# Kernel tuning notes

Measured on AMD Instinct MI355X. Metric: run time of the kernel, lower is better.

Reference implementation:

```python
import jax, jax.numpy as jnp
import numpy as np

B, T, C, H, NC = 512, 256, 512, 512, 96  # batch, encoder steps, channels, hidden, num classes


def setup_inputs() -> dict:
    key = jax.random.key(0)
    ks = jax.random.split(key, 12)
    def w(k, shape, fan):
        return (jax.random.normal(k, shape, jnp.float32) / np.sqrt(fan)).astype(jnp.float32)
    labels = jax.random.randint(ks[0], (B,), 0, NC)
    return {
        "prev_h": jax.random.normal(ks[1], (B, H), jnp.float32),
        "prev_c": jax.random.normal(ks[2], (B, H), jnp.float32),
        "batch_H": jax.random.normal(ks[3], (B, T, C), jnp.float32),
        "char_onehots": jax.nn.one_hot(labels, NC, dtype=jnp.float32),
        "Wi": w(ks[4], (C, H), C),            # i2h kernel (no bias)
        "Wh": w(ks[5], (H, H), H),            # h2h kernel
        "bh": jnp.zeros((H,), jnp.float32),    # h2h bias
        "Ws": w(ks[6], (H, 1), H),            # score kernel (no bias)
        "K": w(ks[7], (C + NC, 4 * H), C + NC),  # LSTM input kernel (i,f,g,o)
        "R": w(ks[8], (H, 4 * H), H),            # LSTM recurrent kernel
        "b": jnp.zeros((4 * H,), jnp.float32),    # LSTM bias
    }


def reference(prev_h, prev_c, batch_H, char_onehots, Wi, Wh, bh, Ws, K, R, b):
    # Additive (Bahdanau) attention
    proj = jnp.einsum('btc,ch->bth', batch_H, Wi)                  # [B,T,H]
    hp = prev_h @ Wh + bh                                          # [B,H]
    e = jnp.einsum('bth,h->bt', jnp.tanh(proj + hp[:, None, :]), Ws[:, 0])  # [B,T]
    alpha = jax.nn.softmax(e, axis=1)                              # [B,T]
    context = jnp.einsum('bt,btc->bc', alpha, batch_H)             # [B,C]
    # LSTMCell step (keras gate order: i, f, g, o; sigmoid recurrent act, tanh act)
    x = jnp.concatenate([context, char_onehots], axis=1)           # [B,C+NC]
    z = x @ K + prev_h @ R + b                                     # [B,4H]
    i, f, g, o = jnp.split(z, 4, axis=1)
    c_new = jax.nn.sigmoid(f) * prev_c + jax.nn.sigmoid(i) * jnp.tanh(g)
    h_new = jax.nn.sigmoid(o) * jnp.tanh(c_new)
    return (h_new, c_new, alpha[:, :, None])  # ((h,c), alpha[B,T,1])
```

## Files before the change

### kernel.cpp

```cpp
#include <hip/hip_runtime.h>
#include <hip/hip_bf16.h>
#include <stdint.h>

#define KFULL 1120
#define N4H   2048
#define MTOT  131072

typedef float f32x4 __attribute__((ext_vector_type(4)));
typedef __bf16 bf16x8 __attribute__((ext_vector_type(8)));
typedef unsigned short u16;
typedef unsigned short ush8 __attribute__((ext_vector_type(8)));

__device__ __forceinline__ u16 f2bf(float f){
  union { float f; unsigned u; } v; v.f = f;
  unsigned u = v.u;
  u += 0x7fffu + ((u >> 16) & 1u);
  return (u16)(u >> 16);
}
__device__ __forceinline__ float sigf(float x){ return 1.f / (1.f + __expf(-x)); }
__device__ __forceinline__ float tanh_fast(float x){ return 1.f - 2.f / (__expf(2.f * x) + 1.f); }
__device__ __forceinline__ int swz(int row){ return (row ^ (row >> 2)) & 3; }

__global__ void prep_w(const float* __restrict__ Wi, const float* __restrict__ Wh,
                       const float* __restrict__ Km, const float* __restrict__ R,
                       u16* __restrict__ wiT, u16* __restrict__ whT, u16* __restrict__ wfT){
  int idx = blockIdx.x * 256 + threadIdx.x;
  if (idx < 524288){
    const float* src = (idx < 262144) ? Wi : Wh;
    u16* dst = (idx < 262144) ? wiT : whT;
    int e = idx & 262143;
    int n = e & 511, kk = (e >> 9) & 31, s = e >> 14;
    float v = src[(size_t)(s * 32 + kk) * 512 + n];
    int dkk = (kk & 7) | ((((kk >> 3) ^ swz(n)) & 3) << 3);
    dst[((size_t)s * 512 + n) * 32 + dkk] = f2bf(v);
  } else {
    int e = idx - 524288;
    if (e >= 35 * 2048 * 32) return;
    int n = e & 2047, kk = (e >> 11) & 31, s = e >> 16;
    int k = s * 32 + kk;
    float v = (k < 608) ? Km[(size_t)k * 2048 + n] : R[(size_t)(k - 608) * 2048 + n];
    int dkk = (kk & 7) | ((((kk >> 3) ^ swz(n)) & 3) << 3);
    wfT[((size_t)s * 2048 + n) * 32 + dkk] = f2bf(v);
  }
}

__global__ void prep_x(const float* __restrict__ onehots, const float* __restrict__ prev_h,
                       float* __restrict__ x_full){
  int idx = blockIdx.x * 256 + threadIdx.x;
  if (idx >= 512 * 608) return;
  int b = idx / 608, c = idx % 608;
  float v = (c < 96) ? onehots[b * 96 + c] : prev_h[b * 512 + (c - 96)];
  x_full[(size_t)b * KFULL + 512 + c] = v;
}

template<int EPI>
__launch_bounds__(256, 3)
__global__ void gemm128(const float* __restrict__ A, int lda, int ksteps,
                        const u16* __restrict__ Bt, int ntot,
                        float* __restrict__ outp, size_t partStride,
                        const float* __restrict__ hpart, const float* __restrict__ bh,
                        const float* __restrict__ Ws, float* __restrict__ epart){
  __shared__ u16 smA[2][128 * 32];
  __shared__ u16 smB[2][128 * 32];
  __shared__ float smHp[128];
  __shared__ float smWs[128];
  __shared__ float smRed[2][128];

  const int tid  = threadIdx.x;
  const int lane = tid & 63, w = tid >> 6;
  const int wr = w >> 1, wc = w & 1;
  const int fr = lane & 15, g = lane >> 4;

  int m0, n0, s0;
  if (EPI == 1){
    int bid = blockIdx.x;
    int sw = (bid & 7) * 512 + (bid >> 3);
    m0 = (sw >> 2) * 128;
    n0 = (sw & 3) * 128;
    s0 = 0;
  } else {
    m0 = blockIdx.x * 128;
    n0 = blockIdx.y * 128;
    s0 = blockIdx.z * ksteps;
    outp += (size_t)blockIdx.z * partStride;
  }

  if (EPI == 1 && tid < 128){
    int b = m0 >> 8;
    float h = bh[n0 + tid];
    #pragma unroll
    for (int p = 0; p < 4; ++p) h += hpart[(size_t)p * 262144 + (size_t)b * 512 + n0 + tid];
    smHp[tid] = h;
    smWs[tid] = Ws[n0 + tid];
  }

  f32x4 acc[4][4] = {};

  const int ar = tid >> 2;
  const int ac = (tid & 3) * 8;
  const float* ap = A + (size_t)(m0 + ar) * lda + ac;
  const int sz  = swz(ar);
  const int ab0 = ar * 64 + (((tid & 3) ^ sz) << 4);
  const int ab1 = ab0 + 64 * 64;

  float4 a0, a1, a2, a3;

#define ISSUE_B(sabs, c) do {                                              \
    const char* bsrc = (const char*)Bt + ((size_t)(sabs) * ntot + n0) * 64;\
    _Pragma("unroll")                                                      \
    for (int j = 0; j < 2; ++j){                                           \
      int off = w * 2048 + j * 1024;                                       \
      __builtin_amdgcn_global_load_lds(                                    \
        (const __attribute__((address_space(1))) void*)(bsrc + off + lane * 16), \
        (__attribute__((address_space(3))) void*)((char*)&smB[c][0] + off),\
        16, 0, 0);                                                         \
    }                                                                      \
  } while(0)

#define LOAD_A(s) do {                                                     \
    int kc = (s0 + (s)) * 32;                                              \
    a0 = *(const float4*)(ap + kc);                                        \
    a1 = *(const float4*)(ap + kc + 4);                                    \
    a2 = *(const float4*)(ap + (size_t)64 * lda + kc);                     \
    a3 = *(const float4*)(ap + (size_t)64 * lda + kc + 4);                 \
  } while(0)

#define WRITE_A(c) do {                                                    \
    ush8 w0, w1;                                                           \
    w0[0]=f2bf(a0.x); w0[1]=f2bf(a0.y); w0[2]=f2bf(a0.z); w0[3]=f2bf(a0.w);\
    w0[4]=f2bf(a1.x); w0[5]=f2bf(a1.y); w0[6]=f2bf(a1.z); w0[7]=f2bf(a1.w);\
    w1[0]=f2bf(a2.x); w1[1]=f2bf(a2.y); w1[2]=f2bf(a2.z); w1[3]=f2bf(a2.w);\
    w1[4]=f2bf(a3.x); w1[5]=f2bf(a3.y); w1[6]=f2bf(a3.z); w1[7]=f2bf(a3.w);\
    *(ush8*)((char*)&smA[c][0] + ab0) = w0;                                \
    *(ush8*)((char*)&smA[c][0] + ab1) = w1;                                \
  } while(0)

#define COMPUTE(c) do {                                                    \
    bf16x8 af[4];                                                          \
    _Pragma("unroll")                                                      \
    for (int m = 0; m < 4; ++m){                                           \
      int rl = wr * 64 + m * 16 + fr;                                      \
      af[m] = *(const bf16x8*)((const char*)&smA[c][0] + rl * 64 + ((g ^ swz(rl)) << 4)); \
    }                                                                      \
    _Pragma("unroll")                                                      \
    for (int n = 0; n < 4; ++n){                                           \
      int nl = wc * 64 + n * 16 + fr;                                      \
      bf16x8 bfv = *(const bf16x8*)((const char*)&smB[c][0] + nl * 64 + ((g ^ swz(nl)) << 4)); \
      _Pragma("unroll")                                                    \
      for (int m = 0; m < 4; ++m)                                          \
        acc[m][n] = __builtin_amdgcn_mfma_f32_16x16x32_bf16(af[m], bfv, acc[m][n], 0, 0, 0); \
    }                                                                      \
  } while(0)

  ISSUE_B(s0, 0);
  LOAD_A(0);
  WRITE_A(0);
  __syncthreads();

  int c = 0;
  for (int s = 0; s < ksteps - 1; ++s){
    ISSUE_B(s0 + s + 1, c ^ 1);
    LOAD_A(s + 1);
    COMPUTE(c);
    WRITE_A(c ^ 1);
    __syncthreads();
    c ^= 1;
  }
  COMPUTE(c);

#undef ISSUE_B
#undef LOAD_A
#undef WRITE_A
#undef COMPUTE

  if (EPI == 0){
    #pragma unroll
    for (int n = 0; n < 4; ++n){
      int col = n0 + wc * 64 + n * 16 + fr;
      #pragma unroll
      for (int m = 0; m < 4; ++m){
        int row = m0 + wr * 64 + m * 16 + g * 4;
        #pragma unroll
        for (int j = 0; j < 4; ++j)
          outp[(size_t)(row + j) * ntot + col] = acc[m][n][j];
      }
    }
  } else {
    float p[16] = {};
    #pragma unroll
    for (int n = 0; n < 4; ++n){
      int col = wc * 64 + n * 16 + fr;
      float hpv = smHp[col], wsv = smWs[col];
      #pragma unroll
      for (int m = 0; m < 4; ++m)
        #pragma unroll
        for (int j = 0; j < 4; ++j)
          p[m * 4 + j] += tanh_fast(acc[m][n][j] + hpv) * wsv;
    }
    #pragma unroll
    for (int mask = 1; mask < 16; mask <<= 1)
      #pragma unroll
      for (int i = 0; i < 16; ++i)
        p[i] += __shfl_xor(p[i], mask);
    __syncthreads();
    if (fr == 0){
      #pragma unroll
      for (int m = 0; m < 4; ++m)
        #pragma unroll
        for (int j = 0; j < 4; ++j)
          smRed[wc][wr * 64 + m * 16 + g * 4 + j] = p[m * 4 + j];
    }
    __syncthreads();
    if (tid < 128){
      int nb = n0 >> 7;
      epart[(size_t)nb * MTOT + m0 + tid] = smRed[0][tid] + smRed[1][tid];
    }
  }
}

__global__ void ctx_softmax(const float* __restrict__ epart, const float* __restrict__ batch_H,
                            float* __restrict__ x_full, float* __restrict__ alpha_out){
  __shared__ float sa[256];
  __shared__ float red[4], red2[4];
  __shared__ f32x4 sred[8][32];
  int b = blockIdx.x, q = blockIdx.y, tid = threadIdx.x;

  float e = 0.f;
  #pragma unroll
  for (int p = 0; p < 4; ++p) e += epart[(size_t)p * MTOT + b * 256 + tid];
  float m = e;
  #pragma unroll
  for (int mask = 1; mask < 64; mask <<= 1) m = fmaxf(m, __shfl_xor(m, mask));
  int w = tid >> 6;
  if ((tid & 63) == 0) red[w] = m;
  __syncthreads();
  m = fmaxf(fmaxf(red[0], red[1]), fmaxf(red[2], red[3]));
  float ev = __expf(e - m);
  float s = ev;
  #pragma unroll
  for (int mask = 1; mask < 64; mask <<= 1) s += __shfl_xor(s, mask);
  if ((tid & 63) == 0) red2[w] = s;
  __syncthreads();
  s = red2[0] + red2[1] + red2[2] + red2[3];
  float a = ev / s;
  sa[tid] = a;
  if (q == 0) alpha_out[(size_t)b * 256 + tid] = a;
  __syncthreads();

  int c4 = tid & 31, tq = tid >> 5;
  const float4* bhp = (const float4*)(batch_H + (size_t)b * 131072) + (size_t)tq * 32 * 128 + q * 32 + c4;
  f32x4 acc = {0.f, 0.f, 0.f, 0.f};
  #pragma unroll 4
  for (int t = 0; t < 32; ++t){
    float av = sa[tq * 32 + t];
    float4 v = bhp[(size_t)t * 128];
    acc[0] += av * v.x; acc[1] += av * v.y; acc[2] += av * v.z; acc[3] += av * v.w;
  }
  sred[tq][c4] = acc;
  __syncthreads();
  if (tid < 32){
    f32x4 o = sred[0][tid];
    #pragma unroll
    for (int r = 1; r < 8; ++r){
      f32x4 v = sred[r][tid];
      o[0] += v[0]; o[1] += v[1]; o[2] += v[2]; o[3] += v[3];
    }
    float4 st; st.x = o[0]; st.y = o[1]; st.z = o[2]; st.w = o[3];
    *(float4*)(x_full + (size_t)b * KFULL + q * 128 + tid * 4) = st;
  }
}

__global__ void gates_k(const float* __restrict__ zpart, const float* __restrict__ bias,
                        const float* __restrict__ prev_c, float* __restrict__ out){
  int idx = blockIdx.x * 256 + threadIdx.x;
  int b = idx >> 9, h = idx & 511;
  float zi = bias[h], zf = bias[512 + h], zg = bias[1024 + h], zo = bias[1536 + h];
  #pragma unroll
  for (int p = 0; p < 5; ++p){
    const float* zr = zpart + (size_t)p * 1048576 + (size_t)b * N4H;
    zi += zr[h]; zf += zr[512 + h]; zg += zr[1024 + h]; zo += zr[1536 + h];
  }
  float c = sigf(zf) * prev_c[idx] + sigf(zi) * tanh_fast(zg);
  float hn = sigf(zo) * tanh_fast(c);
  out[idx] = hn;
  out[262144 + idx] = c;
}

extern "C" void kernel_launch(void* const* d_in, const int* in_sizes, int n_in,
                              void* d_out, int out_size, void* d_ws, size_t ws_size,
                              hipStream_t stream){
  const float* prev_h  = (const float*)d_in[0];
  const float* prev_c  = (const float*)d_in[1];
  const float* batch_H = (const float*)d_in[2];
  const float* onehots = (const float*)d_in[3];
  const float* Wi      = (const float*)d_in[4];
  const float* Wh      = (const float*)d_in[5];
  const float* bh      = (const float*)d_in[6];
  const float* Ws      = (const float*)d_in[7];
  const float* Km      = (const float*)d_in[8];
  const float* R       = (const float*)d_in[9];
  const float* bb      = (const float*)d_in[10];
  float* out = (float*)d_out;

  char* ws = (char*)d_ws;
  u16*  wiT    = (u16*)(ws + 0);
  u16*  whT    = (u16*)(ws + 524288);
  u16*  wfT    = (u16*)(ws + 1048576);
  float* hpart = (float*)(ws + 5636096);
  float* epart = (float*)(ws + 9830400);
  float* x_full= (float*)(ws + 11927552);
  float* zpart = (float*)(ws + 14221312);

  float* alpha = out + 524288;

  prep_w<<<11008, 256, 0, stream>>>(Wi, Wh, Km, R, wiT, whT, wfT);
  prep_x<<<1216, 256, 0, stream>>>(onehots, prev_h, x_full);
  gemm128<0><<<dim3(4, 4, 4), 256, 0, stream>>>(prev_h, 512, 4, whT, 512,
                                                hpart, 262144, nullptr, nullptr, nullptr, nullptr);
  gemm128<1><<<dim3(4096, 1, 1), 256, 0, stream>>>(batch_H, 512, 16, wiT, 512,
                                                   nullptr, 0, hpart, bh, Ws, epart);
  ctx_softmax<<<dim3(512, 4), 256, 0, stream>>>(epart, batch_H, x_full, alpha);
  gemm128<0><<<dim3(4, 16, 5), 256, 0, stream>>>(x_full, KFULL, 7, wfT, N4H,
                                                 zpart, 1048576, nullptr, nullptr, nullptr, nullptr);
  gates_k<<<1024, 256, 0, stream>>>(zpart, bb, prev_c, out);
}
```

Baseline: 232.7 us.

## Stream fp32 A tiles directly to LDS and convert to bf16 at fragment load

```diff
diff --git a/kernel.cpp b/kernel.cpp
--- a/kernel.cpp
+++ b/kernel.cpp
@@ -9,13 +9,11 @@
 typedef float f32x4 __attribute__((ext_vector_type(4)));
 typedef __bf16 bf16x8 __attribute__((ext_vector_type(8)));
 typedef unsigned short u16;
-typedef unsigned short ush8 __attribute__((ext_vector_type(8)));
-
-__device__ __forceinline__ u16 f2bf(float f){
-  union { float f; unsigned u; } v; v.f = f;
-  unsigned u = v.u;
-  u += 0x7fffu + ((u >> 16) & 1u);
-  return (u16)(u >> 16);
+
+__device__ __forceinline__ u16 f2bf_bits(float f){
+  __bf16 b = (__bf16)f;
+  union { __bf16 b; u16 u; } cv; cv.b = b;
+  return cv.u;
 }
 __device__ __forceinline__ float sigf(float x){ return 1.f / (1.f + __expf(-x)); }
 __device__ __forceinline__ float tanh_fast(float x){ return 1.f - 2.f / (__expf(2.f * x) + 1.f); }
@@ -32,7 +30,7 @@
     int n = e & 511, kk = (e >> 9) & 31, s = e >> 14;
     float v = src[(size_t)(s * 32 + kk) * 512 + n];
     int dkk = (kk & 7) | ((((kk >> 3) ^ swz(n)) & 3) << 3);
-    dst[((size_t)s * 512 + n) * 32 + dkk] = f2bf(v);
+    dst[((size_t)s * 512 + n) * 32 + dkk] = f2bf_bits(v);
   } else {
     int e = idx - 524288;
     if (e >= 35 * 2048 * 32) return;
@@ -40,7 +38,7 @@
     int k = s * 32 + kk;
     float v = (k < 608) ? Km[(size_t)k * 2048 + n] : R[(size_t)(k - 608) * 2048 + n];
     int dkk = (kk & 7) | ((((kk >> 3) ^ swz(n)) & 3) << 3);
-    wfT[((size_t)s * 2048 + n) * 32 + dkk] = f2bf(v);
+    wfT[((size_t)s * 2048 + n) * 32 + dkk] = f2bf_bits(v);
   }
 }
 
@@ -60,8 +58,8 @@
                         float* __restrict__ outp, size_t partStride,
                         const float* __restrict__ hpart, const float* __restrict__ bh,
                         const float* __restrict__ Ws, float* __restrict__ epart){
-  __shared__ u16 smA[2][128 * 32];
-  __shared__ u16 smB[2][128 * 32];
+  __shared__ float smA[2][128 * 32];
+  __shared__ u16   smB[2][128 * 32];
   __shared__ float smHp[128];
   __shared__ float smWs[128];
   __shared__ float smRed[2][128];
@@ -93,19 +91,29 @@
     smHp[tid] = h;
     smWs[tid] = Ws[n0 + tid];
   }
+  asm volatile("s_waitcnt vmcnt(0) lgkmcnt(0)" ::: "memory");
 
   f32x4 acc[4][4] = {};
 
-  const int ar = tid >> 2;
-  const int ac = (tid & 3) * 8;
-  const float* ap = A + (size_t)(m0 + ar) * lda + ac;
-  const int sz  = swz(ar);
-  const int ab0 = ar * 64 + (((tid & 3) ^ sz) << 4);
-  const int ab1 = ab0 + 64 * 64;
-
-  float4 a0, a1, a2, a3;
-
-#define ISSUE_B(sabs, c) do {                                              \
+  const int arow = lane >> 3;
+  const int achk = (lane & 7) ^ arow;
+  const char* abase = (const char*)A + ((size_t)(m0 + w * 8 + arow) * lda) * 4 + achk * 16;
+  const size_t aRowStride32 = (size_t)32 * lda * 4;
+  const int aLdsBase = (w * 8) * 128;
+
+  const int fsw = fr & 7;
+  const int a_c0 = ((2 * g) ^ fsw) << 4;
+  const int a_c1 = ((2 * g + 1) ^ fsw) << 4;
+
+#define ISSUE_AB(sabs, c) do {                                             \
+    const char* as = abase + (size_t)(sabs) * 32 * 4;                      \
+    _Pragma("unroll")                                                      \
+    for (int j = 0; j < 4; ++j){                                           \
+      __builtin_amdgcn_global_load_lds(                                    \
+        (const __attribute__((address_space(1))) void*)(as + j * aRowStride32), \
+        (__attribute__((address_space(3))) void*)((char*)&smA[c][0] + aLdsBase + j * 4096), \
+        16, 0, 0);                                                         \
+    }                                                                      \
     const char* bsrc = (const char*)Bt + ((size_t)(sabs) * ntot + n0) * 64;\
     _Pragma("unroll")                                                      \
     for (int j = 0; j < 2; ++j){                                           \
@@ -117,30 +125,17 @@
     }                                                                      \
   } while(0)
 
-#define LOAD_A(s) do {                                                     \
-    int kc = (s0 + (s)) * 32;                                              \
-    a0 = *(const float4*)(ap + kc);                                        \
-    a1 = *(const float4*)(ap + kc + 4);                                    \
-    a2 = *(const float4*)(ap + (size_t)64 * lda + kc);                     \
-    a3 = *(const float4*)(ap + (size_t)64 * lda + kc + 4);                 \
-  } while(0)
-
-#define WRITE_A(c) do {                                                    \
-    ush8 w0, w1;                                                           \
-    w0[0]=f2bf(a0.x); w0[1]=f2bf(a0.y); w0[2]=f2bf(a0.z); w0[3]=f2bf(a0.w);\
-    w0[4]=f2bf(a1.x); w0[5]=f2bf(a1.y); w0[6]=f2bf(a1.z); w0[7]=f2bf(a1.w);\
-    w1[0]=f2bf(a2.x); w1[1]=f2bf(a2.y); w1[2]=f2bf(a2.z); w1[3]=f2bf(a2.w);\
-    w1[4]=f2bf(a3.x); w1[5]=f2bf(a3.y); w1[6]=f2bf(a3.z); w1[7]=f2bf(a3.w);\
-    *(ush8*)((char*)&smA[c][0] + ab0) = w0;                                \
-    *(ush8*)((char*)&smA[c][0] + ab1) = w1;                                \
-  } while(0)
-
 #define COMPUTE(c) do {                                                    \
     bf16x8 af[4];                                                          \
     _Pragma("unroll")                                                      \
     for (int m = 0; m < 4; ++m){                                           \
       int rl = wr * 64 + m * 16 + fr;                                      \
-      af[m] = *(const bf16x8*)((const char*)&smA[c][0] + rl * 64 + ((g ^ swz(rl)) << 4)); \
+      f32x4 lo = *(const f32x4*)((const char*)&smA[c][0] + rl * 128 + a_c0); \
+      f32x4 hi = *(const f32x4*)((const char*)&smA[c][0] + rl * 128 + a_c1); \
+      af[m][0] = (__bf16)lo[0]; af[m][1] = (__bf16)lo[1];                  \
+      af[m][2] = (__bf16)lo[2]; af[m][3] = (__bf16)lo[3];                  \
+      af[m][4] = (__bf16)hi[0]; af[m][5] = (__bf16)hi[1];                  \
+      af[m][6] = (__bf16)hi[2]; af[m][7] = (__bf16)hi[3];                  \
     }                                                                      \
     _Pragma("unroll")                                                      \
     for (int n = 0; n < 4; ++n){                                           \
@@ -152,25 +147,25 @@
     }                                                                      \
   } while(0)
 
-  ISSUE_B(s0, 0);
-  LOAD_A(0);
-  WRITE_A(0);
-  __syncthreads();
-
-  int c = 0;
-  for (int s = 0; s < ksteps - 1; ++s){
-    ISSUE_B(s0 + s + 1, c ^ 1);
-    LOAD_A(s + 1);
-    COMPUTE(c);
-    WRITE_A(c ^ 1);
-    __syncthreads();
-    c ^= 1;
-  }
-  COMPUTE(c);
-
-#undef ISSUE_B
-#undef LOAD_A
-#undef WRITE_A
+  ISSUE_AB(s0, 0);
+
+  for (int s = 0; s < ksteps; ++s){
+    const int cur = s & 1;
+    if (s + 1 < ksteps){
+      ISSUE_AB(s0 + s + 1, cur ^ 1);
+      asm volatile("s_waitcnt vmcnt(6)" ::: "memory");
+    } else {
+      asm volatile("s_waitcnt vmcnt(0)" ::: "memory");
+    }
+    __builtin_amdgcn_s_barrier();
+    asm volatile("" ::: "memory");
+    COMPUTE(cur);
+    asm volatile("" ::: "memory");
+    __builtin_amdgcn_s_barrier();
+    asm volatile("" ::: "memory");
+  }
+
+#undef ISSUE_AB
 #undef COMPUTE
 
   if (EPI == 0){
@@ -202,7 +197,6 @@
       #pragma unroll
       for (int i = 0; i < 16; ++i)
         p[i] += __shfl_xor(p[i], mask);
-    __syncthreads();
     if (fr == 0){
       #pragma unroll
       for (int m = 0; m < 4; ++m)
```

Measured after the change: 224.6 us. 1.04x faster.
